# Kernel optimization log

Measured on AMD Instinct MI355X. Metric: run time of the kernel, lower is better.

## Reference

```python
import jax, jax.numpy as jnp
import numpy as np

DT = 0.01  # time_delta from init
SIGMA, RHO, BETA = 10.0, 28.0, 8.0 / 3.0  # Lorenz parameters for self.function


def setup_inputs() -> dict:
    key = jax.random.key(0)
    # traj: [T, len_var, B] ensemble of trajectory states over time
    traj = jax.random.normal(key, (2048, 3, 8192), dtype=jnp.float32)
    return {"traj": traj}


def _jacobian(state):
    # state: [V, B] -> discrete tangent map I + DT * J_lorenz(state), shape [B, V, V]
    x, y, z = state[0], state[1], state[2]
    zero = jnp.zeros_like(x)
    one = jnp.ones_like(x)
    J = jnp.stack([
        jnp.stack([-SIGMA * one, SIGMA * one, zero], axis=-1),
        jnp.stack([RHO - z, -one, -x], axis=-1),
        jnp.stack([y, x, -BETA * one], axis=-1),
    ], axis=-2)  # [B, V, V]
    return jnp.eye(3, dtype=state.dtype) + DT * J


def _gram_schmidt_rows(M):
    # Row-wise Gram-Schmidt + normalization, exactly as the torch gram_schmidt
    # (in-place slicing makes it modified GS against already-orthogonalized rows)
    # followed by normalization(). M: [B, V, V]. Returns (Q [B,V,V], lognorms [V,B]).
    V = M.shape[-2]
    rows, lognorms = [], []
    for k in range(V):
        r = M[..., k, :]
        for q in rows:  # q already unit-norm -> projection coeff is just q.r
            r = r - jnp.sum(q * r, axis=-1, keepdims=True) * q
        n = jnp.sqrt(jnp.sum(r * r, axis=-1, keepdims=True))
        rows.append(r / n)
        lognorms.append(jnp.log(n[..., 0]))
    return jnp.stack(rows, axis=-2), jnp.stack(lognorms, axis=0)


def reference(traj):
    T, V, B = traj.shape
    Q0 = jnp.broadcast_to(jnp.eye(V, dtype=traj.dtype), (B, V, V))

    def step(Q, state):
        M = jnp.einsum('bij,bjk->bik', _jacobian(state), Q)  # eye = Jaco @ eye
        Qn, ln = _gram_schmidt_rows(M)
        return Qn, ln

    _, lns = jax.lax.scan(step, Q0, traj)  # lns: [T, V, B]
    # Running-average recurrence L_{k+1} = (L_k*k*dt + log n_k)/((k+1)*dt)
    # telescopes exactly to sum_k log(n_k) / (T * dt).
    return jnp.sum(lns, axis=0) / (T * DT)  # [V, B] Lyapunov spectrum per trajectory
```

## Files before the change

### kernel.cpp

```cpp
#include <hip/hip_runtime.h>

#define T_STEPS 2048
#define B_CH    8192
#define DT_F    0.01f
#define NCHUNK  64
#define CHUNK   (T_STEPS / NCHUNK)
#define WARM    32
#define TILE    4

typedef float v2f __attribute__((ext_vector_type(2)));

__device__ __forceinline__ float fast_rsqrt(float x) { return __builtin_amdgcn_rsqf(x); }
__device__ __forceinline__ float fast_log2(float x)  { return __builtin_amdgcn_logf(x); }
__device__ __forceinline__ v2f v2_rsq(v2f n) {
  v2f r; r.x = fast_rsqrt(n.x); r.y = fast_rsqrt(n.y); return r;
}

struct Q9 { v2f q00,q01,q02,q10,q11,q12,q20,q21,q22; };

__device__ __forceinline__ void gs_step(v2f x, v2f y, v2f z, Q9& Q,
                                        v2f& P0, v2f& P1, v2f& P2) {
  const float a00 = 0.9f;
  const float a01 = 0.1f;
  const float a11 = 0.99f;
  const float a22 = 1.0f - DT_F * (8.0f / 3.0f);
  v2f a10 = DT_F * (28.0f - z);
  v2f a12 = -DT_F * x;
  v2f a20 = DT_F * y;
  v2f a21 = DT_F * x;

  v2f m00 = a00*Q.q00 + a01*Q.q10;
  v2f m01 = a00*Q.q01 + a01*Q.q11;
  v2f m02 = a00*Q.q02 + a01*Q.q12;
  v2f m10 = a10*Q.q00 + a11*Q.q10 + a12*Q.q20;
  v2f m11 = a10*Q.q01 + a11*Q.q11 + a12*Q.q21;
  v2f m12 = a10*Q.q02 + a11*Q.q12 + a12*Q.q22;
  v2f m20 = a20*Q.q00 + a21*Q.q10 + a22*Q.q20;
  v2f m21 = a20*Q.q01 + a21*Q.q11 + a22*Q.q21;
  v2f m22 = a20*Q.q02 + a21*Q.q12 + a22*Q.q22;

  v2f n0 = m00*m00 + m01*m01 + m02*m02;
  v2f d1 = m00*m10 + m01*m11 + m02*m12;
  v2f d2 = m00*m20 + m01*m21 + m02*m22;

  v2f i0 = v2_rsq(n0);
  v2f inv0 = i0 * i0;
  P0 *= n0;
  Q.q00 = m00*i0; Q.q01 = m01*i0; Q.q02 = m02*i0;

  v2f c1 = d1 * inv0;
  v2f r10 = m10 - c1*m00, r11 = m11 - c1*m01, r12 = m12 - c1*m02;
  v2f c2 = d2 * inv0;
  v2f r20 = m20 - c2*m00, r21 = m21 - c2*m01, r22 = m22 - c2*m02;

  v2f n1 = r10*r10 + r11*r11 + r12*r12;
  v2f d3 = r10*r20 + r11*r21 + r12*r22;
  v2f i1 = v2_rsq(n1);
  v2f inv1 = i1 * i1;
  P1 *= n1;
  Q.q10 = r10*i1; Q.q11 = r11*i1; Q.q12 = r12*i1;

  v2f c3 = d3 * inv1;
  v2f s20 = r20 - c3*r10, s21 = r21 - c3*r11, s22 = r22 - c3*r12;
  v2f n2 = s20*s20 + s21*s21 + s22*s22;
  v2f i2 = v2_rsq(n2);
  P2 *= n2;
  Q.q20 = s20*i2; Q.q21 = s21*i2; Q.q22 = s22*i2;
}

__global__ __launch_bounds__(256) void lyap_chunk_kernel(const float* __restrict__ traj,
                                                         float* __restrict__ ws) {
  const int c = blockIdx.x * 256 + threadIdx.x;
  const int chunk = blockIdx.y;
  const int warm = (chunk == 0) ? 0 : WARM;
  const int warmPer = warm / (2 * TILE);
  const int nper = (CHUNK + warm) / (2 * TILE);
  const int R = B_CH / 2;
  const v2f* __restrict__ p =
      (const v2f*)traj + (size_t)(chunk * CHUNK - warm) * (3 * R) + c;

  v2f sA[TILE][3], sB[TILE][3];
#pragma unroll
  for (int i = 0; i < TILE; ++i) {
    sA[i][0] = p[(i*3 + 0) * R];
    sA[i][1] = p[(i*3 + 1) * R];
    sA[i][2] = p[(i*3 + 2) * R];
  }

  Q9 Q;
  Q.q00 = 1.f; Q.q01 = 0.f; Q.q02 = 0.f;
  Q.q10 = 0.f; Q.q11 = 1.f; Q.q12 = 0.f;
  Q.q20 = 0.f; Q.q21 = 0.f; Q.q22 = 1.f;
  v2f S0 = 0.f, S1 = 0.f, S2 = 0.f;
  v2f B0 = 0.f, B1 = 0.f, B2 = 0.f;
  v2f P0 = 1.f, P1 = 1.f, P2 = 1.f;

  for (int per = 0; per < nper; ++per) {
    if (per == warmPer) { B0 = S0; B1 = S1; B2 = S2; }
    {
      const v2f* pt = p + (size_t)(2*per + 1) * (TILE * 3 * R);
#pragma unroll
      for (int i = 0; i < TILE; ++i) {
        sB[i][0] = pt[(i*3 + 0) * R];
        sB[i][1] = pt[(i*3 + 1) * R];
        sB[i][2] = pt[(i*3 + 2) * R];
      }
    }
#pragma unroll
    for (int i = 0; i < TILE; ++i)
      gs_step(sA[i][0], sA[i][1], sA[i][2], Q, P0, P1, P2);

    if (per + 1 < nper) {
      const v2f* pt = p + (size_t)(2*per + 2) * (TILE * 3 * R);
#pragma unroll
      for (int i = 0; i < TILE; ++i) {
        sA[i][0] = pt[(i*3 + 0) * R];
        sA[i][1] = pt[(i*3 + 1) * R];
        sA[i][2] = pt[(i*3 + 2) * R];
      }
    }
#pragma unroll
    for (int i = 0; i < TILE; ++i)
      gs_step(sB[i][0], sB[i][1], sB[i][2], Q, P0, P1, P2);

    S0.x += fast_log2(P0.x); S0.y += fast_log2(P0.y); P0 = 1.f;
    S1.x += fast_log2(P1.x); S1.y += fast_log2(P1.y); P1 = 1.f;
    S2.x += fast_log2(P2.x); S2.y += fast_log2(P2.y); P2 = 1.f;
  }

  v2f* __restrict__ wsv = (v2f*)ws;
  wsv[(chunk*3 + 0) * R + c] = S0 - B0;
  wsv[(chunk*3 + 1) * R + c] = S1 - B1;
  wsv[(chunk*3 + 2) * R + c] = S2 - B2;
}

__global__ __launch_bounds__(256) void lyap_reduce_kernel(const float* __restrict__ ws,
                                                          float* __restrict__ out) {
  const int i = blockIdx.x * 256 + threadIdx.x;
  float s = 0.f;
#pragma unroll
  for (int c = 0; c < NCHUNK; ++c) s += ws[c * 3 * B_CH + i];
  const float scale = 0.5f * 0.69314718055994531f / (T_STEPS * DT_F);
  out[i] = s * scale;
}

extern "C" void kernel_launch(void* const* d_in, const int* in_sizes, int n_in,
                              void* d_out, int out_size, void* d_ws, size_t ws_size,
                              hipStream_t stream) {
  (void)in_sizes; (void)n_in; (void)out_size; (void)ws_size;
  const float* traj = (const float*)d_in[0];
  float* out = (float*)d_out;
  float* ws  = (float*)d_ws;

  lyap_chunk_kernel<<<dim3(B_CH / 512, NCHUNK), dim3(256), 0, stream>>>(traj, ws);
  lyap_reduce_kernel<<<dim3(3 * B_CH / 256), dim3(256), 0, stream>>>(ws, out);
}
```

Measured before the change: 295.3 us.

## Replace sequential Gram-Schmidt recurrence with closed-form per-step Gram determinants

Because each Q is orthogonal, the row norms from Gram-Schmidt of J·Q equal those of J alone. So the first log-norm is a constant, the product of the first two squared norms is the Gram determinant of J's first two rows, and the product of all three is det(J) squared. The kernel now computes these per-step quantities directly from the state, with no carried Q and no Gram-Schmidt. The time axis is split into many independent slices, and a reduce kernel recovers the three exponents from the summed logs. This removes the serial dependency and most of the arithmetic, turning the kernel into a streaming read of the trajectory. It relies on hardcoded constants and accumulates products over 8 steps before taking the log.

```diff
diff --git a/kernel.cpp b/kernel.cpp
--- a/kernel.cpp
+++ b/kernel.cpp
@@ -1,147 +1,83 @@
 #include <hip/hip_runtime.h>
+
 
 #define T_STEPS 2048
 #define B_CH    8192
 #define DT_F    0.01f
-#define NCHUNK  64
-#define CHUNK   (T_STEPS / NCHUNK)
-#define WARM    32
-#define TILE    4
+#define SLICES  256
+#define SPT     (T_STEPS / SLICES)
+#define QUADS   (B_CH / 4)
 
 typedef float v2f __attribute__((ext_vector_type(2)));
+typedef float v4f __attribute__((ext_vector_type(4)));
 
-__device__ __forceinline__ float fast_rsqrt(float x) { return __builtin_amdgcn_rsqf(x); }
-__device__ __forceinline__ float fast_log2(float x)  { return __builtin_amdgcn_logf(x); }
-__device__ __forceinline__ v2f v2_rsq(v2f n) {
-  v2f r; r.x = fast_rsqrt(n.x); r.y = fast_rsqrt(n.y); return r;
+__device__ __forceinline__ float fast_log2(float x) { return __builtin_amdgcn_logf(x); }
+
+__device__ __forceinline__ void step_pair(v2f x, v2f y, v2f z, v2f& P1, v2f& PD) {
+  const float INV082 = 1.2195122f;
+  v2f a10 = 0.28f - DT_F * z;
+  v2f xx  = x * x;
+  v2f xy  = x * y;
+  v2f n1  = 0.9801f + 1.0e-4f * xx;
+  n1      = n1 + a10 * a10;
+  v2f d1  = 0.099f + 0.9f * a10;
+  v2f t   = d1 * INV082;
+  v2f nr1 = n1 - t * d1;
+  P1 *= nr1;
+  v2f det = 0.86724f - 0.09733333f * a10;
+  det     = det + 9.0e-5f * xx;
+  det     = det - 1.0e-5f * xy;
+  PD *= det;
 }
 
-struct Q9 { v2f q00,q01,q02,q10,q11,q12,q20,q21,q22; };
+__global__ __launch_bounds__(256) void lyap_stream_kernel(const float* __restrict__ traj,
+                                                          float* __restrict__ ws) {
+  const int q = blockIdx.x * 256 + threadIdx.x;
+  const int s = blockIdx.y;
+  const v4f* __restrict__ p =
+      (const v4f*)traj + (size_t)(s * SPT) * (3 * QUADS) + q;
 
-__device__ __forceinline__ void gs_step(v2f x, v2f y, v2f z, Q9& Q,
-                                        v2f& P0, v2f& P1, v2f& P2) {
-  const float a00 = 0.9f;
-  const float a01 = 0.1f;
-  const float a11 = 0.99f;
-  const float a22 = 1.0f - DT_F * (8.0f / 3.0f);
-  v2f a10 = DT_F * (28.0f - z);
-  v2f a12 = -DT_F * x;
-  v2f a20 = DT_F * y;
-  v2f a21 = DT_F * x;
-
-  v2f m00 = a00*Q.q00 + a01*Q.q10;
-  v2f m01 = a00*Q.q01 + a01*Q.q11;
-  v2f m02 = a00*Q.q02 + a01*Q.q12;
-  v2f m10 = a10*Q.q00 + a11*Q.q10 + a12*Q.q20;
-  v2f m11 = a10*Q.q01 + a11*Q.q11 + a12*Q.q21;
-  v2f m12 = a10*Q.q02 + a11*Q.q12 + a12*Q.q22;
-  v2f m20 = a20*Q.q00 + a21*Q.q10 + a22*Q.q20;
-  v2f m21 = a20*Q.q01 + a21*Q.q11 + a22*Q.q21;
-  v2f m22 = a20*Q.q02 + a21*Q.q12 + a22*Q.q22;
-
-  v2f n0 = m00*m00 + m01*m01 + m02*m02;
-  v2f d1 = m00*m10 + m01*m11 + m02*m12;
-  v2f d2 = m00*m20 + m01*m21 + m02*m22;
-
-  v2f i0 = v2_rsq(n0);
-  v2f inv0 = i0 * i0;
-  P0 *= n0;
-  Q.q00 = m00*i0; Q.q01 = m01*i0; Q.q02 = m02*i0;
-
-  v2f c1 = d1 * inv0;
-  v2f r10 = m10 - c1*m00, r11 = m11 - c1*m01, r12 = m12 - c1*m02;
-  v2f c2 = d2 * inv0;
-  v2f r20 = m20 - c2*m00, r21 = m21 - c2*m01, r22 = m22 - c2*m02;
-
-  v2f n1 = r10*r10 + r11*r11 + r12*r12;
-  v2f d3 = r10*r20 + r11*r21 + r12*r22;
-  v2f i1 = v2_rsq(n1);
-  v2f inv1 = i1 * i1;
-  P1 *= n1;
-  Q.q10 = r10*i1; Q.q11 = r11*i1; Q.q12 = r12*i1;
-
-  v2f c3 = d3 * inv1;
-  v2f s20 = r20 - c3*r10, s21 = r21 - c3*r11, s22 = r22 - c3*r12;
-  v2f n2 = s20*s20 + s21*s21 + s22*s22;
-  v2f i2 = v2_rsq(n2);
-  P2 *= n2;
-  Q.q20 = s20*i2; Q.q21 = s21*i2; Q.q22 = s22*i2;
-}
-
-__global__ __launch_bounds__(256) void lyap_chunk_kernel(const float* __restrict__ traj,
-                                                         float* __restrict__ ws) {
-  const int c = blockIdx.x * 256 + threadIdx.x;
-  const int chunk = blockIdx.y;
-  const int warm = (chunk == 0) ? 0 : WARM;
-  const int warmPer = warm / (2 * TILE);
-  const int nper = (CHUNK + warm) / (2 * TILE);
-  const int R = B_CH / 2;
-  const v2f* __restrict__ p =
-      (const v2f*)traj + (size_t)(chunk * CHUNK - warm) * (3 * R) + c;
-
-  v2f sA[TILE][3], sB[TILE][3];
+  v2f P1a = 1.f, P1b = 1.f, PDa = 1.f, PDb = 1.f;
 #pragma unroll
-  for (int i = 0; i < TILE; ++i) {
-    sA[i][0] = p[(i*3 + 0) * R];
-    sA[i][1] = p[(i*3 + 1) * R];
-    sA[i][2] = p[(i*3 + 2) * R];
+  for (int i = 0; i < SPT; ++i) {
+    v4f X = p[(i * 3 + 0) * QUADS];
+    v4f Y = p[(i * 3 + 1) * QUADS];
+    v4f Z = p[(i * 3 + 2) * QUADS];
+    v2f xa = {X.x, X.y}, xb = {X.z, X.w};
+    v2f ya = {Y.x, Y.y}, yb = {Y.z, Y.w};
+    v2f za = {Z.x, Z.y}, zb = {Z.z, Z.w};
+    step_pair(xa, ya, za, P1a, PDa);
+    step_pair(xb, yb, zb, P1b, PDb);
   }
 
-  Q9 Q;
-  Q.q00 = 1.f; Q.q01 = 0.f; Q.q02 = 0.f;
-  Q.q10 = 0.f; Q.q11 = 1.f; Q.q12 = 0.f;
-  Q.q20 = 0.f; Q.q21 = 0.f; Q.q22 = 1.f;
-  v2f S0 = 0.f, S1 = 0.f, S2 = 0.f;
-  v2f B0 = 0.f, B1 = 0.f, B2 = 0.f;
-  v2f P0 = 1.f, P1 = 1.f, P2 = 1.f;
+  v4f h1, hD;
+  h1.x = fast_log2(P1a.x); h1.y = fast_log2(P1a.y);
+  h1.z = fast_log2(P1b.x); h1.w = fast_log2(P1b.y);
+  hD.x = fast_log2(PDa.x); hD.y = fast_log2(PDa.y);
+  hD.z = fast_log2(PDb.x); hD.w = fast_log2(PDb.y);
 
-  for (int per = 0; per < nper; ++per) {
-    if (per == warmPer) { B0 = S0; B1 = S1; B2 = S2; }
-    {
-      const v2f* pt = p + (size_t)(2*per + 1) * (TILE * 3 * R);
-#pragma unroll
-      for (int i = 0; i < TILE; ++i) {
-        sB[i][0] = pt[(i*3 + 0) * R];
-        sB[i][1] = pt[(i*3 + 1) * R];
-        sB[i][2] = pt[(i*3 + 2) * R];
-      }
-    }
-#pragma unroll
-    for (int i = 0; i < TILE; ++i)
-      gs_step(sA[i][0], sA[i][1], sA[i][2], Q, P0, P1, P2);
-
-    if (per + 1 < nper) {
-      const v2f* pt = p + (size_t)(2*per + 2) * (TILE * 3 * R);
-#pragma unroll
-      for (int i = 0; i < TILE; ++i) {
-        sA[i][0] = pt[(i*3 + 0) * R];
-        sA[i][1] = pt[(i*3 + 1) * R];
-        sA[i][2] = pt[(i*3 + 2) * R];
-      }
-    }
-#pragma unroll
-    for (int i = 0; i < TILE; ++i)
-      gs_step(sB[i][0], sB[i][1], sB[i][2], Q, P0, P1, P2);
-
-    S0.x += fast_log2(P0.x); S0.y += fast_log2(P0.y); P0 = 1.f;
-    S1.x += fast_log2(P1.x); S1.y += fast_log2(P1.y); P1 = 1.f;
-    S2.x += fast_log2(P2.x); S2.y += fast_log2(P2.y); P2 = 1.f;
-  }
-
-  v2f* __restrict__ wsv = (v2f*)ws;
-  wsv[(chunk*3 + 0) * R + c] = S0 - B0;
-  wsv[(chunk*3 + 1) * R + c] = S1 - B1;
-  wsv[(chunk*3 + 2) * R + c] = S2 - B2;
+  v4f* __restrict__ w1 = (v4f*)ws;
+  v4f* __restrict__ wD = w1 + SLICES * QUADS;
+  w1[s * QUADS + q] = h1;
+  wD[s * QUADS + q] = hD;
 }
 
 __global__ __launch_bounds__(256) void lyap_reduce_kernel(const float* __restrict__ ws,
                                                           float* __restrict__ out) {
-  const int i = blockIdx.x * 256 + threadIdx.x;
-  float s = 0.f;
-#pragma unroll
-  for (int c = 0; c < NCHUNK; ++c) s += ws[c * 3 * B_CH + i];
-  const float scale = 0.5f * 0.69314718055994531f / (T_STEPS * DT_F);
-  out[i] = s * scale;
+  const int c = blockIdx.x * 256 + threadIdx.x;
+  const float* __restrict__ w1 = ws;
+  const float* __restrict__ wD = ws + (size_t)SLICES * B_CH;
+  float H1 = 0.f, HD = 0.f;
+#pragma unroll 8
+  for (int s = 0; s < SLICES; ++s) {
+    H1 += w1[s * B_CH + c];
+    HD += wD[s * B_CH + c];
+  }
+  const float scale = 0.5f * 0.69314718f / (T_STEPS * DT_F);
+  const float LAM0  = -9.9225470f;
+  out[c]            = LAM0;
+  out[B_CH + c]     = scale * H1;
+  out[2 * B_CH + c] = scale * (2.f * HD - H1) - LAM0;
 }
 
 extern "C" void kernel_launch(void* const* d_in, const int* in_sizes, int n_in,
@@ -152,6 +88,6 @@
   float* out = (float*)d_out;
   float* ws  = (float*)d_ws;
 
-  lyap_chunk_kernel<<<dim3(B_CH / 512, NCHUNK), dim3(256), 0, stream>>>(traj, ws);
-  lyap_reduce_kernel<<<dim3(3 * B_CH / 256), dim3(256), 0, stream>>>(ws, out);
+  lyap_stream_kernel<<<dim3(QUADS / 256, SLICES), dim3(256), 0, stream>>>(traj, ws);
+  lyap_reduce_kernel<<<dim3(B_CH / 256), dim3(256), 0, stream>>>(ws, out);
 }
```

Measured after the change: 282.5 us. 4.3% less time.
